# Performance work log

Measured on AMD Instinct MI355X. Metric: run time of the kernel, lower is better.

## Reference

```python
import jax, jax.numpy as jnp
import numpy as np
import math

TAU = 0.04
BIG = 100000.0


def _decay(initial, step, steps):
    de = initial * 0.75 * (1.0 + math.cos(math.pi * step / (steps / 2.0)))
    dm = initial * 0.75 * (1.0 + math.cos(math.pi * step / steps))
    e = de if step < steps / 2.0 else 0.0
    m = dm
    return e, m, 3.0 - e - m


def _normalize(x):
    return x / jnp.maximum(jnp.linalg.norm(x, axis=1, keepdims=True), 1e-12)


def _pdist(a2, b2, ab):
    # ||a_i||^2 + ||b_j||^2 - 2 a_i.b_j, clamped + sqrt (matches torch addmm_ path)
    return jnp.sqrt(jnp.clip(a2 + b2.T - 2.0 * ab, 1e-12, None))


def _row_extreme(masked, is_min):
    idx = jnp.argmin(masked, axis=1) if is_min else jnp.argmax(masked, axis=1)
    val = jnp.take_along_axis(masked, idx[:, None], axis=1)[:, 0]
    return val, idx


def _nanmedian(vals, mask):
    # lower-median over valid entries per row (torch.nanmedian semantics)
    k = mask.sum(axis=1)
    pos = jnp.maximum((k - 1) // 2, 0)
    order = jnp.argsort(jnp.where(mask, vals, jnp.inf), axis=1)
    med_idx = jnp.take_along_axis(order, pos[:, None], axis=1)[:, 0]
    med_val = jnp.take_along_axis(vals, med_idx[:, None], axis=1)[:, 0]
    med_val = jnp.where(k > 0, med_val, 0.0)  # NaN-median -> 0 as in source
    return med_val, med_idx


def _ce0(logits):
    # CrossEntropy with labels all 0 over 2 classes
    return jnp.mean(jax.nn.logsumexp(logits, axis=1) - logits[:, 0])


def _pair_loss(dist_vals_an, dist_vals_ap, an_t, ap_t):
    sg = jax.lax.stop_gradient
    w_an = jnp.clip(sg(an_t) - sg(dist_vals_an), 0.0, None)
    w_ap = jnp.clip(sg(dist_vals_ap) - sg(ap_t), 0.0, None)
    logits = jnp.stack([w_an * dist_vals_an / TAU, w_ap * dist_vals_ap / TAU], axis=1)
    return _ce0(logits)


def _forward(teacher_inputs, inputs, epoch):
    e, m, d = _decay(0.5, epoch, 240)
    t = _normalize(teacher_inputs)
    s = _normalize(inputs)
    t2 = jnp.sum(t * t, axis=1, keepdims=True)  # [n,1]
    s2 = jnp.sum(s * s, axis=1, keepdims=True)
    dist_t = _pdist(t2, t2, t @ t.T)            # teacher-teacher [n,n]
    dist = _pdist(t2, s2, t @ s.T)              # teacher-student [n,n]
    temp1 = jnp.diag(dist)[:, None]             # dist[i,i] broadcast over row i
    neg_mask = dist_t > temp1
    pos_mask = ~neg_mask

    gather_t = lambda idx: jnp.take_along_axis(dist_t, idx[:, None], axis=1)[:, 0]

    # hard mining (d-branch): nearest negative, farthest positive
    an_v, an_i = _row_extreme(jnp.where(neg_mask, dist, BIG), True)
    ap_v, ap_i = _row_extreme(jnp.where(pos_mask, dist, 0.0), False)
    loss_d = _pair_loss(an_v, ap_v, gather_t(an_i), gather_t(ap_i))

    # easy mining (e-branch): farthest negative, nearest positive
    an_ev, an_ei = _row_extreme(jnp.where(neg_mask, dist, 0.0), False)
    ap_ev, ap_ei = _row_extreme(jnp.where(pos_mask, dist, BIG), True)
    loss_e = _pair_loss(an_ev, ap_ev, gather_t(an_ei), gather_t(ap_ei))

    # median mining (m-branch)
    an_mv, an_mi = _nanmedian(dist, neg_mask)
    ap_mv, ap_mi = _nanmedian(dist, pos_mask)
    loss_m = _pair_loss(an_mv, ap_mv, gather_t(an_mi), gather_t(ap_mi))

    return loss_e * e + loss_m * m + loss_d * d


def setup_inputs() -> dict:
    key = jax.random.key(0)
    k1, k2 = jax.random.split(key)
    n, dim = 4096, 2048
    return {
        "teacher_inputs": jax.random.normal(k1, (n, dim), dtype=jnp.float32),
        "inputs": jax.random.normal(k2, (n, dim), dtype=jnp.float32),
        "epoch": 100,
    }


def reference(teacher_inputs, inputs, epoch):
    return _forward(teacher_inputs, inputs, epoch)
```

## Files before the change

kernel.cpp:

```cpp
#include <hip/hip_runtime.h>
#include <math.h>
#include <cfloat>
#include <climits>

#define NROW 4096
#define DIM  2048
#define BIGF 100000.0f
#define BIGU 0x47C35000u

typedef float  f32x4  __attribute__((ext_vector_type(4)));
typedef __bf16 bf16x8 __attribute__((ext_vector_type(8)));
typedef unsigned short us8v __attribute__((ext_vector_type(8)));

__device__ __forceinline__ unsigned short f2bf(float x) {
    unsigned u = __float_as_uint(x);
    u += 0x7fffu + ((u >> 16) & 1u);
    return (unsigned short)(u >> 16);
}
__device__ __forceinline__ float bf2f(unsigned short h) {
    return __uint_as_float(((unsigned)h) << 16);
}

__device__ __forceinline__ void gload16(const void* g, void* lds) {
    __builtin_amdgcn_global_load_lds(
        (const __attribute__((address_space(1))) unsigned int*)g,
        (__attribute__((address_space(3))) unsigned int*)lds,
        16, 0, 0);
}

__global__ __launch_bounds__(256) void k_norm_split(
    const float* __restrict__ t_in, const float* __restrict__ s_in,
    unsigned short* __restrict__ T1, unsigned short* __restrict__ T2,
    unsigned short* __restrict__ S1, unsigned short* __restrict__ S2,
    float* __restrict__ t2v, float* __restrict__ s2v)
{
    int b   = blockIdx.x;
    int row = b & (NROW - 1);
    bool isS = b >= NROW;
    const float* in = isS ? s_in : t_in;
    unsigned short* hi = isS ? S1 : T1;
    unsigned short* lo = isS ? S2 : T2;
    float* sq = isS ? s2v : t2v;

    int tid = threadIdx.x;
    const float4* rp = (const float4*)(in + (size_t)row * DIM);
    float4 v0 = rp[tid * 2 + 0];
    float4 v1 = rp[tid * 2 + 1];
    float ss = v0.x*v0.x + v0.y*v0.y + v0.z*v0.z + v0.w*v0.w
             + v1.x*v1.x + v1.y*v1.y + v1.z*v1.z + v1.w*v1.w;
    #pragma unroll
    for (int off = 32; off > 0; off >>= 1) ss += __shfl_down(ss, off, 64);
    __shared__ float wsum[4];
    __shared__ float s_den;
    if ((tid & 63) == 0) wsum[tid >> 6] = ss;
    __syncthreads();
    if (tid == 0) {
        float tot = wsum[0] + wsum[1] + wsum[2] + wsum[3];
        float den = fmaxf(sqrtf(tot), 1e-12f);
        s_den = den;
        sq[row] = tot / (den * den);
    }
    __syncthreads();
    float den = s_den;
    float xs[8];
    xs[0]=v0.x/den; xs[1]=v0.y/den; xs[2]=v0.z/den; xs[3]=v0.w/den;
    xs[4]=v1.x/den; xs[5]=v1.y/den; xs[6]=v1.z/den; xs[7]=v1.w/den;
    us8v hv, lv;
    #pragma unroll
    for (int j = 0; j < 8; ++j) {
        unsigned short h = f2bf(xs[j]);
        hv[j] = h;
        lv[j] = f2bf(xs[j] - bf2f(h));
    }
    *(us8v*)&hi[(size_t)row * DIM + tid * 8] = hv;
    *(us8v*)&lo[(size_t)row * DIM + tid * 8] = lv;
}

__global__ __launch_bounds__(256, 2) void k_gemm_mfma(
    const unsigned short* __restrict__ T1, const unsigned short* __restrict__ T2,
    const unsigned short* __restrict__ S1, const unsigned short* __restrict__ S2,
    const float* __restrict__ t2v, const float* __restrict__ s2v,
    float* __restrict__ distT, float* __restrict__ distS)
{
    __shared__ __align__(16) unsigned char smem[3][24576];

    int tid = threadIdx.x;

    int orig  = blockIdx.y * gridDim.x + blockIdx.x;
    int nwg   = gridDim.x * gridDim.y;
    int cpx   = nwg >> 3;
    int swz   = (orig & 7) * cpx + (orig >> 3);
    int bx    = swz % gridDim.x;
    int by    = swz / gridDim.x;
    int m0 = by * 128, n0 = bx * 128;

    int r0   = tid >> 2;
    int cs0  = (((tid & 3) ^ ((r0 >> 1) & 3)) << 4);
    unsigned ldst = (unsigned)tid * 16;

    size_t offA0 = ((size_t)(m0 + r0)      * DIM) * 2 + cs0;
    size_t offA1 = ((size_t)(m0 + 64 + r0) * DIM) * 2 + cs0;
    size_t offB0 = ((size_t)(n0 + r0)      * DIM) * 2 + cs0;
    size_t offB1 = ((size_t)(n0 + 64 + r0) * DIM) * 2 + cs0;

    int l  = tid & 63;
    int w  = tid >> 6;
    int wr = w >> 1, wc = w & 1;
    int lr = l & 15;
    int kc = l >> 4;

    f32x4 acc_t[4][4], acc_s[4][4];
    #pragma unroll
    for (int m = 0; m < 4; ++m)
        #pragma unroll
        for (int n = 0; n < 4; ++n) {
            acc_t[m][n] = (f32x4)0.0f;
            acc_s[m][n] = (f32x4)0.0f;
        }

    const char* cT1 = (const char*)T1;
    const char* cT2 = (const char*)T2;
    const char* cS1 = (const char*)S1;
    const char* cS2 = (const char*)S2;

    auto stage6 = [&](const char* sA, const char* sBt, const char* sBs,
                      int kk, unsigned char* base) {
        size_t kb = (size_t)kk << 6;
        gload16(sA  + offA0 + kb, base + ldst);
        gload16(sA  + offA1 + kb, base + 4096  + ldst);
        gload16(sBt + offB0 + kb, base + 8192  + ldst);
        gload16(sBt + offB1 + kb, base + 12288 + ldst);
        gload16(sBs + offB0 + kb, base + 16384 + ldst);
        gload16(sBs + offB1 + kb, base + 20480 + ldst);
    };

    auto compute_pair = [&](const unsigned char* aBase, const unsigned char* bBase) {
        bf16x8 a[4], btf[4], bsf[4];
        #pragma unroll
        for (int m = 0; m < 4; ++m) {
            int ra = wr * 64 + m * 16 + lr;
            int co = ((kc ^ ((ra >> 1) & 3)) << 4);
            a[m] = *(const bf16x8*)(aBase + ra * 64 + co);
        }
        #pragma unroll
        for (int n = 0; n < 4; ++n) {
            int rb = wc * 64 + n * 16 + lr;
            int co = ((kc ^ ((rb >> 1) & 3)) << 4);
            btf[n] = *(const bf16x8*)(bBase + 8192  + rb * 64 + co);
            bsf[n] = *(const bf16x8*)(bBase + 16384 + rb * 64 + co);
        }
        #pragma unroll
        for (int m = 0; m < 4; ++m)
            #pragma unroll
            for (int n = 0; n < 4; ++n) {
                acc_t[m][n] = __builtin_amdgcn_mfma_f32_16x16x32_bf16(
                    a[m], btf[n], acc_t[m][n], 0, 0, 0);
                acc_s[m][n] = __builtin_amdgcn_mfma_f32_16x16x32_bf16(
                    a[m], bsf[n], acc_s[m][n], 0, 0, 0);
            }
    };

    unsigned char* pP = smem[0];
    unsigned char* pQ = smem[1];
    unsigned char* pN = smem[2];

    stage6(cT1, cT1, cS1, 0, pP);
    __syncthreads();

    for (int k = 0; k < 64; ++k) {
        stage6(cT2, cT2, cS2, k, pQ);
        compute_pair(pP, pP);
        __syncthreads();

        if (k < 63) stage6(cT1, cT1, cS1, k + 1, pN);
        compute_pair(pP, pQ);
        compute_pair(pQ, pP);
        __syncthreads();

        unsigned char* t0 = pQ; pQ = pP; pP = pN; pN = t0;
    }

    int colb = n0 + wc * 64 + lr;
    int rowb = m0 + wr * 64 + (kc << 2);
    float t2row[4][4];
    #pragma unroll
    for (int m = 0; m < 4; ++m)
        #pragma unroll
        for (int r = 0; r < 4; ++r) t2row[m][r] = t2v[rowb + m * 16 + r];
    #pragma unroll
    for (int n = 0; n < 4; ++n) {
        int col = colb + n * 16;
        float t2c = t2v[col];
        float s2c = s2v[col];
        #pragma unroll
        for (int m = 0; m < 4; ++m) {
            f32x4 ct = acc_t[m][n];
            f32x4 cs = acc_s[m][n];
            int row = rowb + m * 16;
            #pragma unroll
            for (int r = 0; r < 4; ++r) {
                size_t o = (size_t)(row + r) * NROW + col;
                distT[o] = sqrtf(fmaxf(t2row[m][r] + t2c - 2.0f * ct[r], 1e-12f));
                distS[o] = sqrtf(fmaxf(t2row[m][r] + s2c - 2.0f * cs[r], 1e-12f));
            }
        }
    }
}

__device__ inline float pair_term(float an_v, float ap_v, float an_t, float ap_t)
{
    float w_an = fmaxf(an_t - an_v, 0.f);
    float w_ap = fmaxf(ap_v - ap_t, 0.f);
    float l0 = w_an * an_v / 0.04f;
    float l1 = w_ap * ap_v / 0.04f;
    float mx = fmaxf(l0, l1);
    return mx + logf(expf(l0 - mx) + expf(l1 - mx)) - l0;
}

__device__ __forceinline__ unsigned long long wred_min64(unsigned long long v) {
    #pragma unroll
    for (int o = 32; o > 0; o >>= 1) {
        unsigned long long x = __shfl_down(v, o, 64);
        v = (x < v) ? x : v;
    }
    return v;
}
__device__ __forceinline__ unsigned long long wred_max64(unsigned long long v) {
    #pragma unroll
    for (int o = 32; o > 0; o >>= 1) {
        unsigned long long x = __shfl_down(v, o, 64);
        v = (x > v) ? x : v;
    }
    return v;
}

__device__ void radix_select_reg(const unsigned u[16], unsigned negbits,
                                 unsigned selNeg, int rank,
                                 unsigned* hist, unsigned* s_wt, unsigned* s_sel,
                                 int tid, float& val, int& idx)
{
    unsigned prefix = 0;
    int r = rank;
    #pragma unroll
    for (int pass = 0; pass < 4; ++pass) {
        const int shift = 24 - pass * 8;
        hist[tid] = 0;
        __syncthreads();
        {
            unsigned curbin = 0xFFFFFFFFu, rl = 0;
            #pragma unroll
            for (int q = 0; q < 16; ++q) {
                unsigned key = (((negbits >> q) & 1u) == selNeg) ? u[q] : 0xFFFFFFFFu;
                bool match = (pass == 0) || ((key >> (shift + 8)) == (prefix >> (shift + 8)));
                if (match) {
                    unsigned b = (key >> shift) & 255u;
                    if (b == curbin) { rl++; }
                    else {
                        if (rl) atomicAdd(&hist[curbin], rl);
                        curbin = b; rl = 1;
                    }
                }
            }
            if (rl) atomicAdd(&hist[curbin], rl);
        }
        __syncthreads();
        unsigned h = hist[tid];
        unsigned incl = h;
        #pragma unroll
        for (int o = 1; o < 64; o <<= 1) {
            unsigned x = __shfl_up(incl, o, 64);
            if ((tid & 63) >= o) incl += x;
        }
        if ((tid & 63) == 63) s_wt[tid >> 6] = incl;
        __syncthreads();
        int wv = tid >> 6;
        unsigned base = 0;
        if (wv > 0) base += s_wt[0];
        if (wv > 1) base += s_wt[1];
        if (wv > 2) base += s_wt[2];
        incl += base;
        unsigned excl = incl - h;
        if ((unsigned)r >= excl && (unsigned)r < incl) {
            s_sel[0] = (unsigned)tid;
            s_sel[1] = (unsigned)r - excl;
        }
        __syncthreads();
        prefix |= s_sel[0] << shift;
        r = (int)s_sel[1];
        __syncthreads();
    }
    {
        unsigned cnt = 0;
        #pragma unroll
        for (int q = 0; q < 16; ++q) {
            unsigned key = (((negbits >> q) & 1u) == selNeg) ? u[q] : 0xFFFFFFFFu;
            if (key == prefix) cnt++;
        }
        hist[tid] = cnt;
        __syncthreads();
        unsigned incl = hist[tid];
        #pragma unroll
        for (int o = 1; o < 64; o <<= 1) {
            unsigned x = __shfl_up(incl, o, 64);
            if ((tid & 63) >= o) incl += x;
        }
        if ((tid & 63) == 63) s_wt[tid >> 6] = incl;
        __syncthreads();
        int wv = tid >> 6;
        unsigned base = 0;
        if (wv > 0) base += s_wt[0];
        if (wv > 1) base += s_wt[1];
        if (wv > 2) base += s_wt[2];
        incl += base;
        unsigned excl = incl - cnt;
        if ((unsigned)r >= excl && (unsigned)r < incl) {
            int need = r - (int)excl;
            #pragma unroll
            for (int q = 0; q < 16; ++q) {
                unsigned key = (((negbits >> q) & 1u) == selNeg) ? u[q] : 0xFFFFFFFFu;
                if (key == prefix) {
                    if (need == 0) { s_sel[0] = (unsigned)(tid * 16 + q); }
                    need--;
                }
            }
        }
        __syncthreads();
    }
    val = __uint_as_float(prefix);
    idx = (int)s_sel[0];
    __syncthreads();
}

__global__ __launch_bounds__(256) void k_rowstats(const float* __restrict__ distS,
    const float* __restrict__ distT, float* __restrict__ terms)
{
    __shared__ unsigned hist[256];
    __shared__ unsigned s_wt[4];
    __shared__ unsigned s_sel[2];
    __shared__ unsigned long long s_red[4][4];
    __shared__ int s_cw[4];
    __shared__ float s_t1;

    int i = blockIdx.x, tid = threadIdx.x;
    const float* dSrow = distS + (size_t)i * NROW;
    const float* dTrow = distT + (size_t)i * NROW;

    if (tid == 0) s_t1 = dSrow[i];

    float4 dv[4], tv[4];
    #pragma unroll
    for (int c = 0; c < 4; ++c) {
        dv[c] = *(const float4*)(dSrow + tid * 16 + c * 4);
        tv[c] = *(const float4*)(dTrow + tid * 16 + c * 4);
    }
    __syncthreads();
    float temp1 = s_t1;

    unsigned u[16];
    unsigned negbits = 0;
    #pragma unroll
    for (int c = 0; c < 4; ++c) {
        const float* dp = (const float*)&dv[c];
        const float* tp = (const float*)&tv[c];
        #pragma unroll
        for (int k = 0; k < 4; ++k) {
            int q = c * 4 + k;
            u[q] = __float_as_uint(dp[k]);
            if (tp[k] > temp1) negbits |= (1u << q);
        }
    }

    unsigned long long Pan  = ~0ull;
    unsigned long long Pap  = 0ull;
    unsigned long long Pane = 0ull;
    unsigned long long Pape = ~0ull;
    int cnt = 0;
    #pragma unroll
    for (int q = 0; q < 16; ++q) {
        unsigned j = (unsigned)(tid * 16 + q);
        unsigned neg = (negbits >> q) & 1u;
        cnt += (int)neg;
        unsigned kan  = neg ? u[q] : BIGU;
        unsigned kap  = neg ? 0u   : u[q];
        unsigned kane = neg ? u[q] : 0u;
        unsigned kape = neg ? BIGU : u[q];
        unsigned long long pan  = ((unsigned long long)kan  << 32) | j;
        unsigned long long pap  = ((unsigned long long)kap  << 32) | (0xFFFFFFFFu - j);
        unsigned long long pane = ((unsigned long long)kane << 32) | (0xFFFFFFFFu - j);
        unsigned long long pape = ((unsigned long long)kape << 32) | j;
        if (pan  < Pan)  Pan  = pan;
        if (pap  > Pap)  Pap  = pap;
        if (pane > Pane) Pane = pane;
        if (pape < Pape) Pape = pape;
    }
    Pan  = wred_min64(Pan);
    Pap  = wred_max64(Pap);
    Pane = wred_max64(Pane);
    Pape = wred_min64(Pape);
    #pragma unroll
    for (int o = 32; o > 0; o >>= 1) cnt += __shfl_down(cnt, o, 64);
    if ((tid & 63) == 0) {
        int wv = tid >> 6;
        s_red[0][wv] = Pan; s_red[1][wv] = Pap;
        s_red[2][wv] = Pane; s_red[3][wv] = Pape;
        s_cw[wv] = cnt;
    }
    __syncthreads();
    unsigned long long Ran = ~0ull, Rap = 0ull, Rane = 0ull, Rape = ~0ull;
    #pragma unroll
    for (int wv = 0; wv < 4; ++wv) {
        if (s_red[0][wv] < Ran)  Ran  = s_red[0][wv];
        if (s_red[1][wv] > Rap)  Rap  = s_red[1][wv];
        if (s_red[2][wv] > Rane) Rane = s_red[2][wv];
        if (s_red[3][wv] < Rape) Rape = s_red[3][wv];
    }
    int k_neg = s_cw[0] + s_cw[1] + s_cw[2] + s_cw[3];
    int k_pos = NROW - k_neg;

    float an_v  = __uint_as_float((unsigned)(Ran  >> 32)); int an_i  = (int)(Ran & 0xFFFFFFFFull);
    float ap_v  = __uint_as_float((unsigned)(Rap  >> 32)); int ap_i  = (int)(0xFFFFFFFFu - (unsigned)(Rap & 0xFFFFFFFFull));
    float ane_v = __uint_as_float((unsigned)(Rane >> 32)); int ane_i = (int)(0xFFFFFFFFu - (unsigned)(Rane & 0xFFFFFFFFull));
    float ape_v = __uint_as_float((unsigned)(Rape >> 32)); int ape_i = (int)(Rape & 0xFFFFFFFFull);

    __syncthreads();

    float mn_v; int mn_i;
    if (k_neg > 0) {
        radix_select_reg(u, negbits, 1u, (k_neg - 1) >> 1, hist, s_wt, s_sel, tid, mn_v, mn_i);
    } else { mn_v = 0.f; mn_i = 0; }
    float mp_v; int mp_i;
    if (k_pos > 0) {
        radix_select_reg(u, negbits, 0u, (k_pos - 1) >> 1, hist, s_wt, s_sel, tid, mp_v, mp_i);
    } else { mp_v = 0.f; mp_i = 0; }

    if (tid == 0) {
        float an_t  = dTrow[an_i];
        float ap_t  = dTrow[ap_i];
        float ane_t = dTrow[ane_i];
        float ape_t = dTrow[ape_i];
        float mn_t  = dTrow[mn_i];
        float mp_t  = dTrow[mp_i];
        terms[i]            = pair_term(an_v,  ap_v,  an_t,  ap_t);
        terms[NROW + i]     = pair_term(ane_v, ape_v, ane_t, ape_t);
        terms[2*NROW + i]   = pair_term(mn_v,  mp_v,  mn_t,  mp_t);
    }
}

__global__ __launch_bounds__(256) void k_finalize(const float* __restrict__ terms,
    const void* __restrict__ epoch_p, float* __restrict__ out)
{
    __shared__ float red[256];
    int tid = threadIdx.x;
    float s0 = 0.f, s1 = 0.f, s2 = 0.f;
    for (int j = tid; j < NROW; j += 256) {
        s0 += terms[j];
        s1 += terms[NROW + j];
        s2 += terms[2*NROW + j];
    }
    float tot[3];
    float sv[3] = {s0, s1, s2};
    for (int t = 0; t < 3; ++t) {
        red[tid] = sv[t];
        __syncthreads();
        for (int st = 128; st > 0; st >>= 1) {
            if (tid < st) red[tid] += red[tid + st];
            __syncthreads();
        }
        tot[t] = red[0];
        __syncthreads();
    }
    if (tid == 0) {
        int ei = *(const int*)epoch_p;
        double step;
        if (ei >= 0 && ei < 100000) step = (double)ei;
        else step = (double)(*(const float*)epoch_p);
        const double PI = 3.14159265358979323846;
        double de = 0.5 * 0.75 * (1.0 + cos(PI * step / 120.0));
        double dm = 0.5 * 0.75 * (1.0 + cos(PI * step / 240.0));
        double e = (step < 120.0) ? de : 0.0;
        double m = dm;
        double d = 3.0 - e - m;
        double loss_d = (double)tot[0] / (double)NROW;
        double loss_e = (double)tot[1] / (double)NROW;
        double loss_m = (double)tot[2] / (double)NROW;
        out[0] = (float)(loss_e * e + loss_m * m + loss_d * d);
    }
}

extern "C" void kernel_launch(void* const* d_in, const int* in_sizes, int n_in,
                              void* d_out, int out_size, void* d_ws, size_t ws_size,
                              hipStream_t stream)
{
    (void)in_sizes; (void)n_in; (void)out_size; (void)ws_size;
    const float* t_in = (const float*)d_in[0];
    const float* s_in = (const float*)d_in[1];
    const void*  epoch = d_in[2];
    float* out = (float*)d_out;

    char* ws = (char*)d_ws;
    size_t off = 0;
    unsigned short* T1 = (unsigned short*)(ws + off); off += (size_t)NROW * DIM * 2;
    unsigned short* T2 = (unsigned short*)(ws + off); off += (size_t)NROW * DIM * 2;
    unsigned short* S1 = (unsigned short*)(ws + off); off += (size_t)NROW * DIM * 2;
    unsigned short* S2 = (unsigned short*)(ws + off); off += (size_t)NROW * DIM * 2;
    float* t2v   = (float*)(ws + off); off += (size_t)NROW * 4;
    float* s2v   = (float*)(ws + off); off += (size_t)NROW * 4;
    float* distT = (float*)(ws + off); off += (size_t)NROW * NROW * 4;
    float* distS = (float*)(ws + off); off += (size_t)NROW * NROW * 4;
    float* terms = (float*)(ws + off); off += (size_t)3 * NROW * 4;

    k_norm_split<<<2 * NROW, 256, 0, stream>>>(t_in, s_in, T1, T2, S1, S2, t2v, s2v);
    k_gemm_mfma<<<dim3(32, 32), 256, 0, stream>>>(T1, T2, S1, S2, t2v, s2v, distT, distS);
    k_rowstats<<<NROW, 256, 0, stream>>>(distS, distT, terms);
    k_finalize<<<1, 256, 0, stream>>>(terms, epoch, out);
}
```

Baseline: 755.5 us.

## Split fused dual-output GEMM into per-output blocks with higher occupancy

Each GEMM workgroup now computes only one of the teacher-teacher or teacher-student distance tiles, selected from the block index, instead of both at once. The grid doubles and per-block accumulators and LDS halve, so launch bounds rise to three blocks per CU. The three split-bf16 passes become a flat 192-step double-buffered loop. The XCD swizzle places the T and S blocks of the same tile together so the shared A tile can be reused from L2. The cost is that the A operand is loaded twice across blocks, and the main loop has more barrier steps.

Result: slower. 773.6 us (+2.4%).

```diff
diff --git a/kernel.cpp b/kernel.cpp
--- a/kernel.cpp
+++ b/kernel.cpp
@@ -76,23 +76,28 @@
     *(us8v*)&lo[(size_t)row * DIM + tid * 8] = lv;
 }
 
-__global__ __launch_bounds__(256, 2) void k_gemm_mfma(
+__global__ __launch_bounds__(256, 3) void k_gemm_mfma(
     const unsigned short* __restrict__ T1, const unsigned short* __restrict__ T2,
     const unsigned short* __restrict__ S1, const unsigned short* __restrict__ S2,
     const float* __restrict__ t2v, const float* __restrict__ s2v,
     float* __restrict__ distT, float* __restrict__ distS)
 {
-    __shared__ __align__(16) unsigned char smem[3][24576];
+    __shared__ __align__(16) unsigned char smem[2][16384];
 
     int tid = threadIdx.x;
 
-    int orig  = blockIdx.y * gridDim.x + blockIdx.x;
-    int nwg   = gridDim.x * gridDim.y;
-    int cpx   = nwg >> 3;
-    int swz   = (orig & 7) * cpx + (orig >> 3);
-    int bx    = swz % gridDim.x;
-    int by    = swz / gridDim.x;
+    int orig = blockIdx.y * gridDim.x + blockIdx.x;
+    int xcd  = orig & 7;
+    int r    = orig >> 3;
+    int zsel = r & 1;
+    int pt   = xcd * 128 + (r >> 1);
+    int bx   = pt & 31, by = pt >> 5;
     int m0 = by * 128, n0 = bx * 128;
+
+    const unsigned short* B1 = zsel ? S1 : T1;
+    const unsigned short* B2 = zsel ? S2 : T2;
+    const float* b2v = zsel ? s2v : t2v;
+    float* outP = zsel ? distS : distT;
 
     int r0   = tid >> 2;
     int cs0  = (((tid & 3) ^ ((r0 >> 1) & 3)) << 4);
@@ -109,75 +114,56 @@
     int lr = l & 15;
     int kc = l >> 4;
 
-    f32x4 acc_t[4][4], acc_s[4][4];
+    f32x4 acc[4][4];
     #pragma unroll
     for (int m = 0; m < 4; ++m)
         #pragma unroll
-        for (int n = 0; n < 4; ++n) {
-            acc_t[m][n] = (f32x4)0.0f;
-            acc_s[m][n] = (f32x4)0.0f;
-        }
-
-    const char* cT1 = (const char*)T1;
-    const char* cT2 = (const char*)T2;
-    const char* cS1 = (const char*)S1;
-    const char* cS2 = (const char*)S2;
-
-    auto stage6 = [&](const char* sA, const char* sBt, const char* sBs,
-                      int kk, unsigned char* base) {
-        size_t kb = (size_t)kk << 6;
-        gload16(sA  + offA0 + kb, base + ldst);
-        gload16(sA  + offA1 + kb, base + 4096  + ldst);
-        gload16(sBt + offB0 + kb, base + 8192  + ldst);
-        gload16(sBt + offB1 + kb, base + 12288 + ldst);
-        gload16(sBs + offB0 + kb, base + 16384 + ldst);
-        gload16(sBs + offB1 + kb, base + 20480 + ldst);
+        for (int n = 0; n < 4; ++n) acc[m][n] = (f32x4)0.0f;
+
+    const int NT = 192;
+
+    auto stage = [&](int tt, unsigned char* base) {
+        int sg = tt >> 6;
+        size_t kb = (size_t)(tt & 63) << 6;
+        const char* pA = (const char*)((sg == 2) ? T2 : T1);
+        const char* pB = (const char*)((sg == 1) ? B2 : B1);
+        gload16(pA + offA0 + kb, base + ldst);
+        gload16(pA + offA1 + kb, base + 4096  + ldst);
+        gload16(pB + offB0 + kb, base + 8192  + ldst);
+        gload16(pB + offB1 + kb, base + 12288 + ldst);
     };
 
-    auto compute_pair = [&](const unsigned char* aBase, const unsigned char* bBase) {
-        bf16x8 a[4], btf[4], bsf[4];
+    auto compute = [&](const unsigned char* base) {
+        bf16x8 a[4], b[4];
         #pragma unroll
         for (int m = 0; m < 4; ++m) {
             int ra = wr * 64 + m * 16 + lr;
             int co = ((kc ^ ((ra >> 1) & 3)) << 4);
-            a[m] = *(const bf16x8*)(aBase + ra * 64 + co);
+            a[m] = *(const bf16x8*)(base + ra * 64 + co);
         }
         #pragma unroll
         for (int n = 0; n < 4; ++n) {
             int rb = wc * 64 + n * 16 + lr;
             int co = ((kc ^ ((rb >> 1) & 3)) << 4);
-            btf[n] = *(const bf16x8*)(bBase + 8192  + rb * 64 + co);
-            bsf[n] = *(const bf16x8*)(bBase + 16384 + rb * 64 + co);
+            b[n] = *(const bf16x8*)(base + 8192 + rb * 64 + co);
         }
         #pragma unroll
         for (int m = 0; m < 4; ++m)
             #pragma unroll
-            for (int n = 0; n < 4; ++n) {
-                acc_t[m][n] = __builtin_amdgcn_mfma_f32_16x16x32_bf16(
-                    a[m], btf[n], acc_t[m][n], 0, 0, 0);
-                acc_s[m][n] = __builtin_amdgcn_mfma_f32_16x16x32_bf16(
-                    a[m], bsf[n], acc_s[m][n], 0, 0, 0);
-            }
+            for (int n = 0; n < 4; ++n)
+                acc[m][n] = __builtin_amdgcn_mfma_f32_16x16x32_bf16(
+                    a[m], b[n], acc[m][n], 0, 0, 0);
     };
 
-    unsigned char* pP = smem[0];
-    unsigned char* pQ = smem[1];
-    unsigned char* pN = smem[2];
-
-    stage6(cT1, cT1, cS1, 0, pP);
-    __syncthreads();
-
-    for (int k = 0; k < 64; ++k) {
-        stage6(cT2, cT2, cS2, k, pQ);
-        compute_pair(pP, pP);
-        __syncthreads();
-
-        if (k < 63) stage6(cT1, cT1, cS1, k + 1, pN);
-        compute_pair(pP, pQ);
-        compute_pair(pQ, pP);
-        __syncthreads();
-
-        unsigned char* t0 = pQ; pQ = pP; pP = pN; pN = t0;
+    stage(0, smem[0]);
+    __syncthreads();
+
+    int cur = 0;
+    for (int t = 0; t < NT; ++t) {
+        if (t + 1 < NT) stage(t + 1, smem[cur ^ 1]);
+        compute(smem[cur]);
+        __syncthreads();
+        cur ^= 1;
     }
 
     int colb = n0 + wc * 64 + lr;
@@ -186,22 +172,19 @@
     #pragma unroll
     for (int m = 0; m < 4; ++m)
         #pragma unroll
-        for (int r = 0; r < 4; ++r) t2row[m][r] = t2v[rowb + m * 16 + r];
+        for (int rr = 0; rr < 4; ++rr) t2row[m][rr] = t2v[rowb + m * 16 + rr];
     #pragma unroll
     for (int n = 0; n < 4; ++n) {
         int col = colb + n * 16;
-        float t2c = t2v[col];
-        float s2c = s2v[col];
+        float b2c = b2v[col];
         #pragma unroll
         for (int m = 0; m < 4; ++m) {
-            f32x4 ct = acc_t[m][n];
-            f32x4 cs = acc_s[m][n];
+            f32x4 c = acc[m][n];
             int row = rowb + m * 16;
             #pragma unroll
-            for (int r = 0; r < 4; ++r) {
-                size_t o = (size_t)(row + r) * NROW + col;
-                distT[o] = sqrtf(fmaxf(t2row[m][r] + t2c - 2.0f * ct[r], 1e-12f));
-                distS[o] = sqrtf(fmaxf(t2row[m][r] + s2c - 2.0f * cs[r], 1e-12f));
+            for (int rr = 0; rr < 4; ++rr) {
+                size_t o = (size_t)(row + rr) * NROW + col;
+                outP[o] = sqrtf(fmaxf(t2row[m][rr] + b2c - 2.0f * c[rr], 1e-12f));
             }
         }
     }
@@ -510,7 +493,7 @@
     float* terms = (float*)(ws + off); off += (size_t)3 * NROW * 4;
 
     k_norm_split<<<2 * NROW, 256, 0, stream>>>(t_in, s_in, T1, T2, S1, S2, t2v, s2v);
-    k_gemm_mfma<<<dim3(32, 32), 256, 0, stream>>>(T1, T2, S1, S2, t2v, s2v, distT, distS);
+    k_gemm_mfma<<<dim3(64, 32), 256, 0, stream>>>(T1, T2, S1, S2, t2v, s2v, distT, distS);
     k_rowstats<<<NROW, 256, 0, stream>>>(distS, distT, terms);
     k_finalize<<<1, 256, 0, stream>>>(terms, epoch, out);
 }
```
